# Performance work log

Hardware: AMD Instinct MI355X
Metric: run time of the kernel (lower is better)

Reference implementation:

```python
import jax, jax.numpy as jnp
import numpy as np

B, T, C = 4, 2048, 1024
H, D = 16, 64  # n_head, head_dim; H*D == C
EPS = 1e-12


def _l2norm(x):
    # matches torch F.normalize(dim=-1): x / max(||x||_2, eps)
    n = jnp.sqrt(jnp.sum(x * x, axis=-1, keepdims=True))
    return x / jnp.maximum(n, EPS)


def setup_inputs() -> dict:
    key = jax.random.key(0)
    ks = jax.random.split(key, 8)
    s = 0.02
    return {
        "x": jax.random.normal(ks[0], (B, T, C), dtype=jnp.float32),
        "Wq": jax.random.normal(ks[1], (C, C), dtype=jnp.float32) * s,
        "Wk": jax.random.normal(ks[2], (C, C), dtype=jnp.float32) * s,
        "Wv": jax.random.normal(ks[3], (C, C), dtype=jnp.float32) * s,
        "Wbeta": jax.random.normal(ks[4], (H, C), dtype=jnp.float32) * s,
        "bbeta": jnp.zeros((H,), dtype=jnp.float32),
        "Wgate": jax.random.normal(ks[5], (C, C), dtype=jnp.float32) * s,
        "Wo": jax.random.normal(ks[6], (C, C), dtype=jnp.float32) * s,
    }


def _forward(x, Wq, Wk, Wv, Wbeta, bbeta, Wgate, Wo):
    q = (x @ Wq.T).reshape(B, T, H, D)
    k = (x @ Wk.T).reshape(B, T, H, D)
    v = (x @ Wv.T).reshape(B, T, H, D)
    beta = jax.nn.sigmoid(x @ Wbeta.T + bbeta)  # (B,T,H)
    gate = jax.nn.sigmoid(x @ Wgate.T)          # (B,T,C)

    q = _l2norm(q)
    k = _l2norm(k)

    # time-major for scan: (T,B,H,D) / (T,B,H)
    qT = jnp.transpose(q, (1, 0, 2, 3))
    kT = jnp.transpose(k, (1, 0, 2, 3))
    vT = jnp.transpose(v, (1, 0, 2, 3))
    bT = jnp.transpose(beta, (1, 0, 2))

    M0 = jnp.zeros((B, H, D, D), dtype=x.dtype)

    def step(M, inp):
        q_t, k_t, v_t, b_t = inp
        o_t = jnp.einsum('bhdc,bhc->bhd', M, q_t)       # read state with q (pre-update)
        Mk = jnp.einsum('bhdc,bhc->bhd', M, k_t)
        dv = v_t - Mk                                    # delta-rule error
        M = M + b_t[..., None, None] * jnp.einsum('bhd,bhc->bhdc', dv, k_t)
        return M, o_t

    _, oT = jax.lax.scan(step, M0, (qT, kT, vT, bT))     # oT: (T,B,H,D)
    o = jnp.transpose(oT, (1, 0, 2, 3)).reshape(B, T, C)
    return (gate * o) @ Wo.T


def reference(x, Wq, Wk, Wv, Wbeta, bbeta, Wgate, Wo):
    return _forward(x, Wq, Wk, Wv, Wbeta, bbeta, Wgate, Wo)
```

## Files before the change

kernel.cpp:

```cpp
#include <hip/hip_runtime.h>
#include <cstdint>
#include <cstddef>

#define Bz 4
#define Tz 2048
#define Cz 1024
#define Hz 16
#define Dz 64
#define NTOK (Bz*Tz)
#define CHL 32
#define NCH (Tz/CHL)

typedef __attribute__((ext_vector_type(8))) short  short8;
typedef __attribute__((ext_vector_type(4))) float  floatx4;

__device__ __forceinline__ unsigned short f2bf(float x) {
  union { float f; uint32_t u; } a; a.f = x;
  uint32_t r = a.u + 0x7fffu + ((a.u >> 16) & 1u);
  return (unsigned short)(r >> 16);
}
__device__ __forceinline__ float bf2f(unsigned short u) {
  union { uint32_t i; float f; } a; a.i = ((uint32_t)u) << 16; return a.f;
}
__device__ __forceinline__ float sigmoidf_(float z) {
  return 1.0f / (1.0f + __expf(-z));
}
__device__ __forceinline__ uint32_t cvtpk_bf16(float a, float b) {
  uint32_t d;
  asm volatile("v_cvt_pk_bf16_f32 %0, %1, %2" : "=v"(d) : "v"(a), "v"(b));
  return d;
}
__device__ __forceinline__ float lo16f(uint32_t u) {
  union { uint32_t i; float f; } a; a.i = u << 16; return a.f;
}
__device__ __forceinline__ float hi16f(uint32_t u) {
  union { uint32_t i; float f; } a; a.i = u & 0xffff0000u; return a.f;
}

__device__ __forceinline__ void gload_lds16(const void* gptr, void* lptr) {
  __builtin_amdgcn_global_load_lds(
      (const __attribute__((address_space(1))) void*)(uintptr_t)gptr,
      (__attribute__((address_space(3))) void*)(uint32_t)(uintptr_t)lptr,
      16, 0, 0);
}

template<int CTRL>
__device__ __forceinline__ float dpp_addf(float x) {
  int y = __builtin_amdgcn_update_dpp(0, __float_as_int(x), CTRL, 0xF, 0xF, true);
  return x + __int_as_float(y);
}
__device__ __forceinline__ float rowsum16(float x) {
  x = dpp_addf<0xB1>(x);
  x = dpp_addf<0x4E>(x);
  x = dpp_addf<0x124>(x);
  x = dpp_addf<0x128>(x);
  return x;
}

union FragU { uint32_t u[4]; short8 s; };

__global__ __launch_bounds__(256) void cvt_bf16_kernel(const float* __restrict__ in,
                                                       unsigned short* __restrict__ out,
                                                       int n4) {
  int i = blockIdx.x * blockDim.x + threadIdx.x;
  int stride = gridDim.x * blockDim.x;
  const float4* in4 = (const float4*)in;
  ushort4* out4 = (ushort4*)out;
  for (; i < n4; i += stride) {
    float4 f = in4[i];
    ushort4 u;
    u.x = f2bf(f.x); u.y = f2bf(f.y); u.z = f2bf(f.z); u.w = f2bf(f.w);
    out4[i] = u;
  }
}

__global__ __launch_bounds__(256) void cvt_w5_kernel(
    const float* __restrict__ s0, const float* __restrict__ s1,
    const float* __restrict__ s2, const float* __restrict__ s3,
    const float* __restrict__ s4,
    unsigned short* __restrict__ d0, unsigned short* __restrict__ d1,
    unsigned short* __restrict__ d2, unsigned short* __restrict__ d3,
    unsigned short* __restrict__ d4, int n4)
{
  const int w = blockIdx.y;
  const float* s = (w == 0) ? s0 : (w == 1) ? s1 : (w == 2) ? s2 : (w == 3) ? s3 : s4;
  unsigned short* d = (w == 0) ? d0 : (w == 1) ? d1 : (w == 2) ? d2 : (w == 3) ? d3 : d4;
  int i = blockIdx.x * blockDim.x + threadIdx.x;
  if (i < n4) {
    float4 f = ((const float4*)s)[i];
    ushort4 u;
    u.x = f2bf(f.x); u.y = f2bf(f.y); u.z = f2bf(f.z); u.w = f2bf(f.w);
    ((ushort4*)d)[i] = u;
  }
}

#define VM8()  asm volatile("s_waitcnt vmcnt(8)" ::: "memory")
#define VM4()  asm volatile("s_waitcnt vmcnt(4)" ::: "memory")
#define VM0()  asm volatile("s_waitcnt vmcnt(0)" ::: "memory")
#define LGKM0() asm volatile("s_waitcnt lgkmcnt(0)" ::: "memory")
#define BARR() __builtin_amdgcn_s_barrier()

__global__ __launch_bounds__(512, 2) void gemm256_kernel(
    const unsigned short* __restrict__ A,
    const unsigned short* __restrict__ W0, const unsigned short* __restrict__ W1,
    const unsigned short* __restrict__ W2, const unsigned short* __restrict__ W3,
    void* __restrict__ O0, void* __restrict__ O1,
    void* __restrict__ O2, void* __restrict__ O3,
    int M, int N, int K, int nz_sigmoid, int norm_mask, int out_bf16)
{
  __shared__ unsigned short smem[8 * 8192];

  const int gx = gridDim.x, gz = gridDim.z;
  const int nwg = gx * gridDim.y * gz;
  int flat = (blockIdx.z * gridDim.y + blockIdx.y) * gx + blockIdx.x;
  if ((nwg & 7) == 0) flat = (flat & 7) * (nwg >> 3) + (flat >> 3);
  const int xz = gx * gz;
  const int by = flat / xz;
  const int rem = flat - by * xz;
  const int bz = rem / gx;
  const int bx = rem - bz * gx;

  const unsigned short* Bw = (bz == 0) ? W0 : (bz == 1) ? W1 : (bz == 2) ? W2 : W3;
  void* Cw = (bz == 0) ? O0 : (bz == 1) ? O1 : (bz == 2) ? O2 : O3;
  const bool act = (bz == nz_sigmoid);
  const bool donorm = (norm_mask >> bz) & 1;

  const int m0 = by * 256, n0 = bx * 256;
  const int tid = threadIdx.x;
  const int wid = tid >> 6, lane = tid & 63;
  const int wm = wid >> 2, wn = wid & 3;
  const int ml = lane & 15, kq = lane >> 4;

  const unsigned short* Ap = A  + (size_t)m0 * K;
  const unsigned short* Bp = Bw + (size_t)n0 * K;

  const int srow = wid * 16 + (lane >> 2);
  const int ss8  = ((lane & 3) ^ ((lane >> 3) & 3)) * 8;
  const int rs8  = (kq ^ ((ml >> 1) & 3)) * 8;
  const int arow = wm * 128 + ml;
  const int brow = wn * 64 + ml;

  const int NT = K >> 6;
  const int hmax = NT << 2;

  floatx4 acc[8][4];
#pragma unroll
  for (int i = 0; i < 8; ++i)
#pragma unroll
    for (int j = 0; j < 4; ++j) acc[i][j] = floatx4{0.f, 0.f, 0.f, 0.f};

#define STAGE1(hsi) do {                                                      \
    const int ht_ = (hsi) >> 2, hh_ = (hsi) & 3;                              \
    const unsigned short* p_ = (hh_ & 1) ? Bp : Ap;                           \
    const int kb_ = ht_ * 64 + (hh_ >> 1) * 32;                               \
    unsigned short* lb_ = &smem[(((ht_ & 1) << 2) + hh_) * 8192 + wid * 512]; \
    gload_lds16(p_ + (size_t)srow * K + kb_ + ss8, lb_);                      \
    gload_lds16(p_ + (size_t)(128 + srow) * K + kb_ + ss8, lb_ + 4096);       \
  } while (0)

  int hs = 0;
  for (; hs < 6 && hs < hmax; ++hs) STAGE1(hs);
  VM8();
  BARR();

#define LOAD_A(Hb, mh)                                                        \
  _Pragma("unroll") for (int i = 0; i < 4; ++i)                               \
    af[i] = *(const short8*)&Hb[(arow + (mh) * 64 + i * 16) * 32 + rs8];
#define LOAD_B(Hb)                                                            \
  _Pragma("unroll") for (int j = 0; j < 4; ++j)                               \
    bf[j] = *(const short8*)&Hb[(brow + j * 16) * 32 + rs8];
#define MFMA_Q(mh)                                                            \
  __builtin_amdgcn_s_setprio(1);                                              \
  _Pragma("unroll") for (int i = 0; i < 4; ++i)                               \
    _Pragma("unroll") for (int j = 0; j < 4; ++j)                             \
      acc[(mh) * 4 + i][j] = __builtin_amdgcn_mfma_f32_16x16x32_bf16(         \
          af[i], bf[j], acc[(mh) * 4 + i][j], 0, 0, 0);                       \
  __builtin_amdgcn_s_setprio(0);
#define STAGE_NEXT() do { if (hs < hmax) { STAGE1(hs); ++hs; } } while (0)

  short8 af[4], bf[4];
  for (int t = 0; t < NT; ++t) {
    const unsigned short* Ah0 = &smem[(((t & 1) << 2) + 0) * 8192];
    const unsigned short* Bh0 = &smem[(((t & 1) << 2) + 1) * 8192];
    const unsigned short* Ah1 = &smem[(((t & 1) << 2) + 2) * 8192];
    const unsigned short* Bh1 = &smem[(((t & 1) << 2) + 3) * 8192];

    LOAD_A(Ah0, 0); LOAD_B(Bh0);
    STAGE_NEXT();
    BARR(); LGKM0();
    MFMA_Q(0);
    BARR();

    LOAD_A(Ah0, 1);
    STAGE_NEXT();
    BARR(); LGKM0();
    MFMA_Q(1);
    if (t == NT - 1) { VM0(); } else { VM8(); }
    BARR();

    LOAD_A(Ah1, 0); LOAD_B(Bh1);
    STAGE_NEXT();
    BARR(); LGKM0();
    MFMA_Q(0);
    BARR();

    LOAD_A(Ah1, 1);
    STAGE_NEXT();
    BARR(); LGKM0();
    MFMA_Q(1);
    if (t < NT - 2) { VM8(); } else if (t == NT - 2) { VM4(); }
    BARR();
  }

  float scale[8][4];
  if (donorm) {
#pragma unroll
    for (int i = 0; i < 8; ++i) {
#pragma unroll
      for (int r = 0; r < 4; ++r) {
        float ss = 0.f;
#pragma unroll
        for (int j = 0; j < 4; ++j) ss = fmaf(acc[i][j][r], acc[i][j][r], ss);
        ss = rowsum16(ss);
        scale[i][r] = 1.0f / fmaxf(sqrtf(ss), 1e-12f);
      }
    }
  }

  const int row_base = m0 + wm * 128;
  const int col_base = n0 + wn * 64;
#pragma unroll
  for (int i = 0; i < 8; ++i) {
#pragma unroll
    for (int j = 0; j < 4; ++j) {
      const int col = col_base + j * 16 + ml;
#pragma unroll
      for (int r = 0; r < 4; ++r) {
        const int row = row_base + i * 16 + kq * 4 + r;
        float val = acc[i][j][r];
        if (donorm) val *= scale[i][r];
        if (act) val = sigmoidf_(val);
        if (out_bf16) ((unsigned short*)Cw)[(size_t)row * N + col] = f2bf(val);
        else          ((float*)Cw)[(size_t)row * N + col] = val;
      }
    }
  }
}

__global__ __launch_bounds__(256) void beta_kernel(
    const float* __restrict__ x, const float* __restrict__ Wb,
    const float* __restrict__ bb, float* __restrict__ beta_out)
{
  const int n = blockIdx.x;
  const int wid = threadIdx.x >> 6;
  const int lane = threadIdx.x & 63;
  const float* xr = x + (size_t)n * Cz;
  for (int h = wid; h < Hz; h += 4) {
    const float* wr = Wb + (size_t)h * Cz;
    float s = 0.f;
#pragma unroll 4
    for (int i = lane; i < Cz; i += 64) s = fmaf(xr[i], wr[i], s);
#pragma unroll
    for (int ofs = 32; ofs >= 1; ofs >>= 1) s += __shfl_xor(s, ofs);
    if (lane == 0) beta_out[(size_t)n * Hz + h] = sigmoidf_(s + bb[h]);
  }
}


__global__ __launch_bounds__(256) void deltachunk_phase1(
    const unsigned short* __restrict__ qb, const unsigned short* __restrict__ kb,
    const unsigned short* __restrict__ vb, const float* __restrict__ betaf,
    float* __restrict__ of,
    unsigned short* __restrict__ qtb, unsigned short* __restrict__ wbuf,
    unsigned short* __restrict__ ubuf, unsigned short* __restrict__ ktb)
{
  __shared__ unsigned short Kb[32][72], Qb[32][72], Vb[32][72];
  __shared__ float As[32][33];
  __shared__ unsigned short Sb[32][40];
  __shared__ unsigned short Us[32][72], Ws[32][72], Qts[32][72];
  __shared__ float bsh[32];

  const int bid = blockIdx.x;
  const int chain = bid & 63;
  const int chunk = bid >> 6;
  const int b = chain >> 4, h = chain & 15;
  const int tid = threadIdx.x;
  const int wid = tid >> 6, lane = tid & 63;
  const int ml = lane & 15, kq = lane >> 4;

  const size_t tok0 = (size_t)b * Tz + (size_t)chunk * CHL;
  const size_t cb = ((size_t)chain * NCH + chunk) * 2048;

  {
    const int row = tid >> 3, c8 = (tid & 7) * 8;
    const size_t ga = (tok0 + row) * Cz + h * Dz + c8;
    *(uint4*)&Qb[row][c8] = *(const uint4*)&qb[ga];
    *(uint4*)&Kb[row][c8] = *(const uint4*)&kb[ga];
    *(uint4*)&Vb[row][c8] = *(const uint4*)&vb[ga];
  }
  if (tid < 32) bsh[tid] = betaf[(tok0 + tid) * Hz + h];
  __syncthreads();

  {
    const int tr = wid & 1, tc = wid >> 1;
    floatx4 accA = {0.f,0.f,0.f,0.f}, accS = {0.f,0.f,0.f,0.f};
#pragma unroll
    for (int eh = 0; eh < 2; ++eh) {
      short8 ka = *(const short8*)&Kb[tr * 16 + ml][eh * 32 + kq * 8];
      short8 kbf = *(const short8*)&Kb[tc * 16 + ml][eh * 32 + kq * 8];
      short8 qa = *(const short8*)&Qb[tr * 16 + ml][eh * 32 + kq * 8];
      accA = __builtin_amdgcn_mfma_f32_16x16x32_bf16(ka, kbf, accA, 0, 0, 0);
      accS = __builtin_amdgcn_mfma_f32_16x16x32_bf16(qa, kbf, accS, 0, 0, 0);
    }
#pragma unroll
    for (int r = 0; r < 4; ++r) {
      int t = tr * 16 + kq * 4 + r;
      int s = tc * 16 + ml;
      As[t][s] = bsh[t] * accA[r];
      Sb[t][s] = (t > s) ? f2bf(accS[r]) : (unsigned short)0;
    }
  }
  __syncthreads();

  if (tid < 128) {
    const int j = tid;
    float x[32];
    if (j < 64) {
#pragma unroll
      for (int t = 0; t < 32; ++t) x[t] = bsh[t] * bf2f(Vb[t][j]);
    } else {
#pragma unroll
      for (int t = 0; t < 32; ++t) x[t] = bsh[t] * bf2f(Kb[t][j - 64]);
    }
#pragma unroll
    for (int t = 0; t < 31; ++t) {
      float xt = x[t];
#pragma unroll
      for (int s = t + 1; s < 32; ++s) x[s] = fmaf(-As[s][t], xt, x[s]);
    }
    if (j < 64) {
#pragma unroll
      for (int t = 0; t < 32; ++t) Us[t][j] = f2bf(x[t]);
    } else {
#pragma unroll
      for (int t = 0; t < 32; ++t) Ws[t][j - 64] = f2bf(x[t]);
    }
  }
  __syncthreads();

  {
    const int dw = wid * 16 + ml;
    FragU bu, bw;
#pragma unroll
    for (int r = 0; r < 4; ++r) {
      bu.u[r] = (uint32_t)Us[kq * 8 + 2 * r][dw] | ((uint32_t)Us[kq * 8 + 2 * r + 1][dw] << 16);
      bw.u[r] = (uint32_t)Ws[kq * 8 + 2 * r][dw] | ((uint32_t)Ws[kq * 8 + 2 * r + 1][dw] << 16);
    }
    floatx4 accO[2], accQ[2];
#pragma unroll
    for (int tt = 0; tt < 2; ++tt) { accO[tt] = floatx4{0.f,0.f,0.f,0.f}; accQ[tt] = floatx4{0.f,0.f,0.f,0.f}; }
#pragma unroll
    for (int tt = 0; tt < 2; ++tt) {
      short8 sa = *(const short8*)&Sb[tt * 16 + ml][kq * 8];
      accO[tt] = __builtin_amdgcn_mfma_f32_16x16x32_bf16(sa, bu.s, accO[tt], 0, 0, 0);
      accQ[tt] = __builtin_amdgcn_mfma_f32_16x16x32_bf16(sa, bw.s, accQ[tt], 0, 0, 0);
    }
#pragma unroll
    for (int tt = 0; tt < 2; ++tt) {
#pragma unroll
      for (int r = 0; r < 4; ++r) {
        int t = tt * 16 + kq * 4 + r;
        of[(tok0 + t) * Cz + h * Dz + dw] = accO[tt][r];
        Qts[t][dw] = f2bf(bf2f(Qb[t][dw]) - accQ[tt][r]);
      }
    }
  }

  unsigned short ktmp[8], utmp[8];
  {
    const int e = tid >> 2, tq = (tid & 3) * 8;
#pragma unroll
    for (int i2 = 0; i2 < 8; ++i2) { ktmp[i2] = Kb[tq + i2][e]; utmp[i2] = Us[tq + i2][e]; }
  }
  __syncthreads();

  {
    const int row = tid >> 3, c8 = (tid & 7) * 8;
    const size_t o16 = cb + (size_t)row * 64 + c8;
    *(uint4*)&qtb[o16]  = *(const uint4*)&Qts[row][c8];
    *(uint4*)&wbuf[o16] = *(const uint4*)&Ws[row][c8];
    const int e = tid >> 2, tq = (tid & 3) * 8;
    *(uint4*)&ktb[cb + (size_t)e * 32 + tq]  = *(const uint4*)ktmp;
    *(uint4*)&ubuf[cb + (size_t)e * 32 + tq] = *(const uint4*)utmp;
  }
}

__global__ __launch_bounds__(256, 1) void deltachunk_phase2(
    const unsigned short* __restrict__ qtb, const unsigned short* __restrict__ wbuf,
    const unsigned short* __restrict__ ubuf, const unsigned short* __restrict__ ktb,
    float* __restrict__ of)
{
  __shared__ unsigned short Gb[2][64][72];
  __shared__ unsigned short Ub[2][64][40];
  __shared__ unsigned short Kts[2][64][40];
  __shared__ unsigned short Mh[2][64][72], Ml[2][64][72];

  const int chain = blockIdx.x;
  const int b = chain >> 4, h = chain & 15;
  const int tid = threadIdx.x;
  const int wid = tid >> 6, lane = tid & 63;
  const int ml = lane & 15, kq = lane >> 4;
  const int iq = wid >> 1, jq = wid & 1;

  for (int i = tid; i < 64 * 72; i += 256) { (&Mh[0][0][0])[i] = 0; (&Ml[0][0][0])[i] = 0; }

  const int g_row = tid >> 2;
  const int g_c0  = (tid & 3) * 16;
  const int k_e   = tid >> 1;
  const int k_c0  = (tid & 1) * 16;

  const size_t cbase = (size_t)chain * NCH * 2048;

  float pre[2][2][4];
  if (iq == 0) {
#pragma unroll
    for (int u = 0; u < 2; ++u) {
      *(uint4*)&Gb[0][g_row][g_c0 + 8*u]    = *(const uint4*)&qtb[cbase + (size_t)g_row * 64 + g_c0 + 8*u];
      *(uint4*)&Gb[0][32 + g_row][g_c0 + 8*u] = *(const uint4*)&wbuf[cbase + (size_t)g_row * 64 + g_c0 + 8*u];
      *(uint4*)&Ub[0][k_e][k_c0 + 8*u]      = *(const uint4*)&ubuf[cbase + (size_t)k_e * 32 + k_c0 + 8*u];
      *(uint4*)&Kts[0][k_e][k_c0 + 8*u]     = *(const uint4*)&ktb[cbase + (size_t)k_e * 32 + k_c0 + 8*u];
    }
    const size_t t0 = (size_t)b * Tz;
#pragma unroll
    for (int ti = 0; ti < 2; ++ti)
#pragma unroll
      for (int tj = 0; tj < 2; ++tj)
#pragma unroll
        for (int r = 0; r < 4; ++r)
          pre[ti][tj][r] = of[(t0 + ti * 16 + kq * 4 + r) * Cz + h * Dz + jq * 32 + tj * 16 + ml];
  }
  __syncthreads();

  const int idxA = ((lane & 15) + 16 * ((2 * kq + 0) & 3)) * 4;
  const int idxB = ((lane & 15) + 16 * ((2 * kq + 1) & 3)) * 4;
  const bool hiKq = (kq >= 2);

  floatx4 mAcc[4][2];
#pragma unroll
  for (int a = 0; a < 4; ++a) { mAcc[a][0] = floatx4{0.f,0.f,0.f,0.f}; mAcc[a][1] = floatx4{0.f,0.f,0.f,0.f}; }

  int cbuf = 0;
  for (int c = 0; c < NCH; ++c) {
    const int nbuf = cbuf ^ 1;
    const int mr = c & 1, mw = mr ^ 1;
    const size_t tok0 = (size_t)b * Tz + (size_t)c * CHL;

    uint4 sq[2], sw[2], su[2], sk[2];
    float preN[2][2][4];
    const int cn = (c + 1 < NCH) ? c + 1 : c;
    if (iq == 0) {
      const size_t cbn = cbase + (size_t)cn * 2048;
#pragma unroll
      for (int u = 0; u < 2; ++u) {
        sq[u] = *(const uint4*)&qtb[cbn + (size_t)g_row * 64 + g_c0 + 8*u];
        sw[u] = *(const uint4*)&wbuf[cbn + (size_t)g_row * 64 + g_c0 + 8*u];
        su[u] = *(const uint4*)&ubuf[cbn + (size_t)k_e * 32 + k_c0 + 8*u];
        sk[u] = *(const uint4*)&ktb[cbn + (size_t)k_e * 32 + k_c0 + 8*u];
      }
      const size_t tkn = (size_t)b * Tz + (size_t)cn * CHL;
#pragma unroll
      for (int ti = 0; ti < 2; ++ti)
#pragma unroll
        for (int tj = 0; tj < 2; ++tj)
#pragma unroll
          for (int r = 0; r < 4; ++r)
            preN[ti][tj][r] = of[(tkn + ti * 16 + kq * 4 + r) * Cz + h * Dz + jq * 32 + tj * 16 + ml];
    }

    floatx4 g1[2][2];
#pragma unroll
    for (int ti = 0; ti < 2; ++ti)
#pragma unroll
      for (int tj = 0; tj < 2; ++tj) g1[ti][tj] = floatx4{0.f,0.f,0.f,0.f};
#pragma unroll
    for (int eh = 0; eh < 2; ++eh) {
      short8 afr0 = *(const short8*)&Gb[cbuf][iq * 32 + 0  + ml][eh * 32 + kq * 8];
      short8 afr1 = *(const short8*)&Gb[cbuf][iq * 32 + 16 + ml][eh * 32 + kq * 8];
#pragma unroll
      for (int hl = 0; hl < 2; ++hl) {
#pragma unroll
        for (int tj = 0; tj < 2; ++tj) {
          short8 bfr = hl ? *(const short8*)&Ml[mr][jq * 32 + tj * 16 + ml][eh * 32 + kq * 8]
                          : *(const short8*)&Mh[mr][jq * 32 + tj * 16 + ml][eh * 32 + kq * 8];
          g1[0][tj] = __builtin_amdgcn_mfma_f32_16x16x32_bf16(afr0, bfr, g1[0][tj], 0, 0, 0);
          g1[1][tj] = __builtin_amdgcn_mfma_f32_16x16x32_bf16(afr1, bfr, g1[1][tj], 0, 0, 0);
        }
      }
    }

    if (iq == 0) {
#pragma unroll
      for (int ti = 0; ti < 2; ++ti)
#pragma unroll
        for (int tj = 0; tj < 2; ++tj)
#pragma unroll
          for (int r = 0; r < 4; ++r)
            of[(tok0 + ti * 16 + kq * 4 + r) * Cz + h * Dz + jq * 32 + tj * 16 + ml] =
                pre[ti][tj][r] + g1[ti][tj][r];
#pragma unroll
      for (int u = 0; u < 2; ++u) {
        *(uint4*)&Gb[nbuf][g_row][g_c0 + 8*u]    = sq[u];
        *(uint4*)&Gb[nbuf][32 + g_row][g_c0 + 8*u] = sw[u];
        *(uint4*)&Ub[nbuf][k_e][k_c0 + 8*u]      = su[u];
        *(uint4*)&Kts[nbuf][k_e][k_c0 + 8*u]     = sk[u];
      }
#pragma unroll
      for (int ti = 0; ti < 2; ++ti)
#pragma unroll
        for (int tj = 0; tj < 2; ++tj)
#pragma unroll
          for (int r = 0; r < 4; ++r) pre[ti][tj][r] = preN[ti][tj][r];
    } else {
      uint32_t pkh[2][2][2], pkl[2][2][2];
#pragma unroll
      for (int ti = 0; ti < 2; ++ti) {
#pragma unroll
        for (int tj = 0; tj < 2; ++tj) {
          const int d = jq * 32 + tj * 16 + ml;
          ushort4 uu = *(const ushort4*)&Ub[cbuf][d][ti * 16 + kq * 4];
          float z0 = bf2f(uu.x) - g1[ti][tj][0];
          float z1 = bf2f(uu.y) - g1[ti][tj][1];
          float z2 = bf2f(uu.z) - g1[ti][tj][2];
          float z3 = bf2f(uu.w) - g1[ti][tj][3];
          uint32_t h01 = cvtpk_bf16(z0, z1), h23 = cvtpk_bf16(z2, z3);
          pkh[ti][tj][0] = h01; pkh[ti][tj][1] = h23;
          pkl[ti][tj][0] = cvtpk_bf16(z0 - lo16f(h01), z1 - hi16f(h01));
          pkl[ti][tj][1] = cvtpk_bf16(z2 - lo16f(h23), z3 - hi16f(h23));
        }
      }
      FragU zh[2], zl[2];
#pragma unroll
      for (int tj = 0; tj < 2; ++tj) {
#pragma unroll
        for (int s = 0; s < 4; ++s) {
          const int idx = (s < 2) ? idxA : idxB;
          const int rp = s & 1;
          int v0 = __builtin_amdgcn_ds_bpermute(idx, (int)pkh[0][tj][rp]);
          int v1 = __builtin_amdgcn_ds_bpermute(idx, (int)pkh[1][tj][rp]);
          zh[tj].u[s] = hiKq ? (uint32_t)v1 : (uint32_t)v0;
          int w0 = __builtin_amdgcn_ds_bpermute(idx, (int)pkl[0][tj][rp]);
          int w1 = __builtin_amdgcn_ds_bpermute(idx, (int)pkl[1][tj][rp]);
          zl[tj].u[s] = hiKq ? (uint32_t)w1 : (uint32_t)w0;
        }
      }
#pragma unroll
      for (int et = 0; et < 4; ++et) {
        short8 kfr = *(const short8*)&Kts[cbuf][et * 16 + ml][kq * 8];
#pragma unroll
        for (int tj = 0; tj < 2; ++tj) {
          mAcc[et][tj] = __builtin_amdgcn_mfma_f32_16x16x32_bf16(kfr, zh[tj].s, mAcc[et][tj], 0, 0, 0);
          mAcc[et][tj] = __builtin_amdgcn_mfma_f32_16x16x32_bf16(kfr, zl[tj].s, mAcc[et][tj], 0, 0, 0);
        }
      }
#pragma unroll
      for (int et = 0; et < 4; ++et) {
#pragma unroll
        for (int tj = 0; tj < 2; ++tj) {
          const int d = jq * 32 + tj * 16 + ml;
          float m0 = mAcc[et][tj][0], m1 = mAcc[et][tj][1];
          float m2 = mAcc[et][tj][2], m3 = mAcc[et][tj][3];
          uint32_t h01 = cvtpk_bf16(m0, m1), h23 = cvtpk_bf16(m2, m3);
          uint32_t l01 = cvtpk_bf16(m0 - lo16f(h01), m1 - hi16f(h01));
          uint32_t l23 = cvtpk_bf16(m2 - lo16f(h23), m3 - hi16f(h23));
          *(uint32_t*)&Mh[mw][d][et * 16 + kq * 4]     = h01;
          *(uint32_t*)&Mh[mw][d][et * 16 + kq * 4 + 2] = h23;
          *(uint32_t*)&Ml[mw][d][et * 16 + kq * 4]     = l01;
          *(uint32_t*)&Ml[mw][d][et * 16 + kq * 4 + 2] = l23;
        }
      }
    }
    __syncthreads();
    cbuf ^= 1;
  }
}

__global__ __launch_bounds__(256) void gate_mul_kernel(
    const unsigned short* __restrict__ gsig, const float* __restrict__ o,
    unsigned short* __restrict__ out, int n4)
{
  int i = blockIdx.x * blockDim.x + threadIdx.x;
  int stride = gridDim.x * blockDim.x;
  const ushort4* g4 = (const ushort4*)gsig;
  const float4* o4 = (const float4*)o;
  ushort4* out4 = (ushort4*)out;
  for (; i < n4; i += stride) {
    ushort4 gv = g4[i];
    float4 ov = o4[i];
    ushort4 u;
    u.x = f2bf(bf2f(gv.x) * ov.x);
    u.y = f2bf(bf2f(gv.y) * ov.y);
    u.z = f2bf(bf2f(gv.z) * ov.z);
    u.w = f2bf(bf2f(gv.w) * ov.w);
    out4[i] = u;
  }
}

extern "C" void kernel_launch(void* const* d_in, const int* in_sizes, int n_in,
                              void* d_out, int out_size, void* d_ws, size_t ws_size,
                              hipStream_t stream) {
  const float* x     = (const float*)d_in[0];
  const float* Wq    = (const float*)d_in[1];
  const float* Wk    = (const float*)d_in[2];
  const float* Wv    = (const float*)d_in[3];
  const float* Wbeta = (const float*)d_in[4];
  const float* bbeta = (const float*)d_in[5];
  const float* Wgate = (const float*)d_in[6];
  const float* Wo    = (const float*)d_in[7];
  float* out = (float*)d_out;

  char* ws = (char*)d_ws;
  size_t off = 0;
  auto alloc = [&](size_t bytes) -> char* {
    char* p = ws + off;
    off += (bytes + 255) & ~(size_t)255;
    return p;
  };
  unsigned short* xb  = (unsigned short*)alloc((size_t)NTOK * Cz * 2);
  unsigned short* Wqb = (unsigned short*)alloc((size_t)Cz * Cz * 2);
  unsigned short* Wkb = (unsigned short*)alloc((size_t)Cz * Cz * 2);
  unsigned short* Wvb = (unsigned short*)alloc((size_t)Cz * Cz * 2);
  unsigned short* Wgb = (unsigned short*)alloc((size_t)Cz * Cz * 2);
  unsigned short* Wob = (unsigned short*)alloc((size_t)Cz * Cz * 2);
  unsigned short* qb  = (unsigned short*)alloc((size_t)NTOK * Cz * 2);
  unsigned short* kb  = (unsigned short*)alloc((size_t)NTOK * Cz * 2);
  unsigned short* vb  = (unsigned short*)alloc((size_t)NTOK * Cz * 2);
  unsigned short* gb  = (unsigned short*)alloc((size_t)NTOK * Cz * 2);
  float* of    = (float*)alloc((size_t)NTOK * Cz * 4);
  float* betaf = (float*)alloc((size_t)NTOK * Hz * 4);
  unsigned short* qtb  = (unsigned short*)alloc((size_t)64 * NCH * 2048 * 2);
  unsigned short* wbuf = (unsigned short*)alloc((size_t)64 * NCH * 2048 * 2);
  unsigned short* ubuf = (unsigned short*)alloc((size_t)64 * NCH * 2048 * 2);
  unsigned short* ktb  = (unsigned short*)alloc((size_t)64 * NCH * 2048 * 2);
  unsigned short* ab = xb;

  const int n4x = NTOK * Cz / 4;
  const int n4w = Cz * Cz / 4;

  cvt_bf16_kernel<<<dim3(1024), dim3(256), 0, stream>>>(x, xb, n4x);
  cvt_w5_kernel<<<dim3(n4w / 256, 5), dim3(256), 0, stream>>>(
      Wq, Wk, Wv, Wgate, Wo, Wqb, Wkb, Wvb, Wgb, Wob, n4w);

  gemm256_kernel<<<dim3(Cz / 256, NTOK / 256, 4), dim3(512), 0, stream>>>(
      xb, Wqb, Wkb, Wvb, Wgb, qb, kb, vb, gb, NTOK, Cz, Cz, 3, 3, 1);

  beta_kernel<<<dim3(NTOK), dim3(256), 0, stream>>>(x, Wbeta, bbeta, betaf);

  deltachunk_phase1<<<dim3(64 * NCH), dim3(256), 0, stream>>>(
      qb, kb, vb, betaf, of, qtb, wbuf, ubuf, ktb);
  deltachunk_phase2<<<dim3(Bz * Hz), dim3(256), 0, stream>>>(qtb, wbuf, ubuf, ktb, of);

  gate_mul_kernel<<<dim3(1024), dim3(256), 0, stream>>>(gb, of, ab, n4x);

  gemm256_kernel<<<dim3(Cz / 256, NTOK / 256, 1), dim3(512), 0, stream>>>(
      ab, Wob, Wob, Wob, Wob, out, out, out, out, NTOK, Cz, Cz, -1, 0, 0);
}
```

Baseline: 411.6 us.

## Split delta-rule state recurrence across value-dim halves and defer intra-chunk add

The sequential chunk-recurrence kernel now runs two blocks per (batch, head) chain, each owning 32 of the 64 value columns of the state, which doubles the parallelism of the serial scan from 64 to 128 blocks. The inter-chunk output contribution is written to a separate buffer instead of a read-modify-write of the intra-chunk output, and the gate kernel sums the two buffers. All threads now share the next-chunk prefetch, and the barrier uses an explicit LDS wait. This adds an extra fp32 activation buffer and more memory traffic in the gate kernel, and it duplicates the Q/W/K loads across the two blocks.

Result: faster. 374.0 us (-9.2%).

```diff
diff --git a/kernel.cpp b/kernel.cpp
--- a/kernel.cpp
+++ b/kernel.cpp
@@ -395,212 +395,158 @@
   }
 }
 
-__global__ __launch_bounds__(256, 1) void deltachunk_phase2(
+__global__ __launch_bounds__(256) void deltachunk_phase2(
     const unsigned short* __restrict__ qtb, const unsigned short* __restrict__ wbuf,
     const unsigned short* __restrict__ ubuf, const unsigned short* __restrict__ ktb,
-    float* __restrict__ of)
+    float* __restrict__ o2)
 {
   __shared__ unsigned short Gb[2][64][72];
-  __shared__ unsigned short Ub[2][64][40];
+  __shared__ unsigned short Ub[2][32][40];
   __shared__ unsigned short Kts[2][64][40];
-  __shared__ unsigned short Mh[2][64][72], Ml[2][64][72];
-
-  const int chain = blockIdx.x;
+  __shared__ unsigned short Mh[2][32][72], Ml[2][32][72];
+
+  const int chain = blockIdx.x >> 1;
+  const int dh = blockIdx.x & 1;
   const int b = chain >> 4, h = chain & 15;
+  const int d0 = dh * 32;
   const int tid = threadIdx.x;
   const int wid = tid >> 6, lane = tid & 63;
   const int ml = lane & 15, kq = lane >> 4;
   const int iq = wid >> 1, jq = wid & 1;
 
-  for (int i = tid; i < 64 * 72; i += 256) { (&Mh[0][0][0])[i] = 0; (&Ml[0][0][0])[i] = 0; }
-
-  const int g_row = tid >> 2;
-  const int g_c0  = (tid & 3) * 16;
-  const int k_e   = tid >> 1;
-  const int k_c0  = (tid & 1) * 16;
-
   const size_t cbase = (size_t)chain * NCH * 2048;
 
-  float pre[2][2][4];
-  if (iq == 0) {
-#pragma unroll
-    for (int u = 0; u < 2; ++u) {
-      *(uint4*)&Gb[0][g_row][g_c0 + 8*u]    = *(const uint4*)&qtb[cbase + (size_t)g_row * 64 + g_c0 + 8*u];
-      *(uint4*)&Gb[0][32 + g_row][g_c0 + 8*u] = *(const uint4*)&wbuf[cbase + (size_t)g_row * 64 + g_c0 + 8*u];
-      *(uint4*)&Ub[0][k_e][k_c0 + 8*u]      = *(const uint4*)&ubuf[cbase + (size_t)k_e * 32 + k_c0 + 8*u];
-      *(uint4*)&Kts[0][k_e][k_c0 + 8*u]     = *(const uint4*)&ktb[cbase + (size_t)k_e * 32 + k_c0 + 8*u];
-    }
-    const size_t t0 = (size_t)b * Tz;
-#pragma unroll
-    for (int ti = 0; ti < 2; ++ti)
-#pragma unroll
-      for (int tj = 0; tj < 2; ++tj)
-#pragma unroll
-        for (int r = 0; r < 4; ++r)
-          pre[ti][tj][r] = of[(t0 + ti * 16 + kq * 4 + r) * Cz + h * Dz + jq * 32 + tj * 16 + ml];
-  }
+  const int grow = tid >> 2;
+  const int gc16 = (tid & 3) * 16;
+  const int ke   = tid >> 2;
+  const int kc8  = (tid & 3) * 8;
+  const int ue   = tid >> 3;
+  const int uc4  = (tid & 7) * 4;
+
+  const unsigned short* gsrc = (grow < 32) ? qtb : wbuf;
+  const size_t gsoff = (size_t)(grow & 31) * 64 + gc16;
+
+  {
+    *(uint4*)&Gb[0][grow][gc16]     = *(const uint4*)&gsrc[cbase + gsoff];
+    *(uint4*)&Gb[0][grow][gc16 + 8] = *(const uint4*)&gsrc[cbase + gsoff + 8];
+    *(uint4*)&Kts[0][ke][kc8]       = *(const uint4*)&ktb[cbase + (size_t)ke * 32 + kc8];
+    *(uint2*)&Ub[0][ue][uc4]        = *(const uint2*)&ubuf[cbase + (size_t)(d0 + ue) * 32 + uc4];
+  }
+  for (int i = tid; i < 32 * 72; i += 256) { (&Mh[0][0][0])[i] = 0; (&Ml[0][0][0])[i] = 0; }
   __syncthreads();
 
-  const int idxA = ((lane & 15) + 16 * ((2 * kq + 0) & 3)) * 4;
-  const int idxB = ((lane & 15) + 16 * ((2 * kq + 1) & 3)) * 4;
+  const int idxA = (ml + 16 * ((kq & 1) * 2)) * 4;
+  const int idxB = (ml + 16 * ((kq & 1) * 2 + 1)) * 4;
   const bool hiKq = (kq >= 2);
 
-  floatx4 mAcc[4][2];
-#pragma unroll
-  for (int a = 0; a < 4; ++a) { mAcc[a][0] = floatx4{0.f,0.f,0.f,0.f}; mAcc[a][1] = floatx4{0.f,0.f,0.f,0.f}; }
-
-  int cbuf = 0;
+  floatx4 mAcc[4];
+#pragma unroll
+  for (int a = 0; a < 4; ++a) mAcc[a] = floatx4{0.f, 0.f, 0.f, 0.f};
+
   for (int c = 0; c < NCH; ++c) {
-    const int nbuf = cbuf ^ 1;
+    const int cbuf = c & 1, nbuf = cbuf ^ 1;
     const int mr = c & 1, mw = mr ^ 1;
     const size_t tok0 = (size_t)b * Tz + (size_t)c * CHL;
 
-    uint4 sq[2], sw[2], su[2], sk[2];
-    float preN[2][2][4];
     const int cn = (c + 1 < NCH) ? c + 1 : c;
-    if (iq == 0) {
-      const size_t cbn = cbase + (size_t)cn * 2048;
-#pragma unroll
-      for (int u = 0; u < 2; ++u) {
-        sq[u] = *(const uint4*)&qtb[cbn + (size_t)g_row * 64 + g_c0 + 8*u];
-        sw[u] = *(const uint4*)&wbuf[cbn + (size_t)g_row * 64 + g_c0 + 8*u];
-        su[u] = *(const uint4*)&ubuf[cbn + (size_t)k_e * 32 + k_c0 + 8*u];
-        sk[u] = *(const uint4*)&ktb[cbn + (size_t)k_e * 32 + k_c0 + 8*u];
-      }
-      const size_t tkn = (size_t)b * Tz + (size_t)cn * CHL;
-#pragma unroll
-      for (int ti = 0; ti < 2; ++ti)
-#pragma unroll
-        for (int tj = 0; tj < 2; ++tj)
-#pragma unroll
-          for (int r = 0; r < 4; ++r)
-            preN[ti][tj][r] = of[(tkn + ti * 16 + kq * 4 + r) * Cz + h * Dz + jq * 32 + tj * 16 + ml];
-    }
-
-    floatx4 g1[2][2];
-#pragma unroll
-    for (int ti = 0; ti < 2; ++ti)
-#pragma unroll
-      for (int tj = 0; tj < 2; ++tj) g1[ti][tj] = floatx4{0.f,0.f,0.f,0.f};
+    const size_t cbn = cbase + (size_t)cn * 2048;
+    uint4 sg0 = *(const uint4*)&gsrc[cbn + gsoff];
+    uint4 sg1 = *(const uint4*)&gsrc[cbn + gsoff + 8];
+    uint4 sk  = *(const uint4*)&ktb[cbn + (size_t)ke * 32 + kc8];
+    uint2 su  = *(const uint2*)&ubuf[cbn + (size_t)(d0 + ue) * 32 + uc4];
+
+    floatx4 g1[2];
+    g1[0] = floatx4{0.f,0.f,0.f,0.f}; g1[1] = floatx4{0.f,0.f,0.f,0.f};
 #pragma unroll
     for (int eh = 0; eh < 2; ++eh) {
       short8 afr0 = *(const short8*)&Gb[cbuf][iq * 32 + 0  + ml][eh * 32 + kq * 8];
       short8 afr1 = *(const short8*)&Gb[cbuf][iq * 32 + 16 + ml][eh * 32 + kq * 8];
-#pragma unroll
-      for (int hl = 0; hl < 2; ++hl) {
-#pragma unroll
-        for (int tj = 0; tj < 2; ++tj) {
-          short8 bfr = hl ? *(const short8*)&Ml[mr][jq * 32 + tj * 16 + ml][eh * 32 + kq * 8]
-                          : *(const short8*)&Mh[mr][jq * 32 + tj * 16 + ml][eh * 32 + kq * 8];
-          g1[0][tj] = __builtin_amdgcn_mfma_f32_16x16x32_bf16(afr0, bfr, g1[0][tj], 0, 0, 0);
-          g1[1][tj] = __builtin_amdgcn_mfma_f32_16x16x32_bf16(afr1, bfr, g1[1][tj], 0, 0, 0);
-        }
+      short8 bh = *(const short8*)&Mh[mr][jq * 16 + ml][eh * 32 + kq * 8];
+      short8 bl = *(const short8*)&Ml[mr][jq * 16 + ml][eh * 32 + kq * 8];
+      g1[0] = __builtin_amdgcn_mfma_f32_16x16x32_bf16(afr0, bh, g1[0], 0, 0, 0);
+      g1[0] = __builtin_amdgcn_mfma_f32_16x16x32_bf16(afr0, bl, g1[0], 0, 0, 0);
+      g1[1] = __builtin_amdgcn_mfma_f32_16x16x32_bf16(afr1, bh, g1[1], 0, 0, 0);
+      g1[1] = __builtin_amdgcn_mfma_f32_16x16x32_bf16(afr1, bl, g1[1], 0, 0, 0);
+    }
+
+    if (iq == 0) {
+#pragma unroll
+      for (int ti = 0; ti < 2; ++ti)
+#pragma unroll
+        for (int r = 0; r < 4; ++r)
+          o2[(tok0 + ti * 16 + kq * 4 + r) * Cz + h * Dz + d0 + jq * 16 + ml] = g1[ti][r];
+    } else {
+      uint32_t pkh[2][2], pkl[2][2];
+#pragma unroll
+      for (int ti = 0; ti < 2; ++ti) {
+        ushort4 uu = *(const ushort4*)&Ub[cbuf][jq * 16 + ml][ti * 16 + kq * 4];
+        float z0 = bf2f(uu.x) - g1[ti][0];
+        float z1 = bf2f(uu.y) - g1[ti][1];
+        float z2 = bf2f(uu.z) - g1[ti][2];
+        float z3 = bf2f(uu.w) - g1[ti][3];
+        uint32_t h01 = cvtpk_bf16(z0, z1), h23 = cvtpk_bf16(z2, z3);
+        pkh[ti][0] = h01; pkh[ti][1] = h23;
+        pkl[ti][0] = cvtpk_bf16(z0 - lo16f(h01), z1 - hi16f(h01));
+        pkl[ti][1] = cvtpk_bf16(z2 - lo16f(h23), z3 - hi16f(h23));
       }
-    }
-
-    if (iq == 0) {
-#pragma unroll
-      for (int ti = 0; ti < 2; ++ti)
-#pragma unroll
-        for (int tj = 0; tj < 2; ++tj)
-#pragma unroll
-          for (int r = 0; r < 4; ++r)
-            of[(tok0 + ti * 16 + kq * 4 + r) * Cz + h * Dz + jq * 32 + tj * 16 + ml] =
-                pre[ti][tj][r] + g1[ti][tj][r];
-#pragma unroll
-      for (int u = 0; u < 2; ++u) {
-        *(uint4*)&Gb[nbuf][g_row][g_c0 + 8*u]    = sq[u];
-        *(uint4*)&Gb[nbuf][32 + g_row][g_c0 + 8*u] = sw[u];
-        *(uint4*)&Ub[nbuf][k_e][k_c0 + 8*u]      = su[u];
-        *(uint4*)&Kts[nbuf][k_e][k_c0 + 8*u]     = sk[u];
-      }
-#pragma unroll
-      for (int ti = 0; ti < 2; ++ti)
-#pragma unroll
-        for (int tj = 0; tj < 2; ++tj)
-#pragma unroll
-          for (int r = 0; r < 4; ++r) pre[ti][tj][r] = preN[ti][tj][r];
-    } else {
-      uint32_t pkh[2][2][2], pkl[2][2][2];
-#pragma unroll
-      for (int ti = 0; ti < 2; ++ti) {
-#pragma unroll
-        for (int tj = 0; tj < 2; ++tj) {
-          const int d = jq * 32 + tj * 16 + ml;
-          ushort4 uu = *(const ushort4*)&Ub[cbuf][d][ti * 16 + kq * 4];
-          float z0 = bf2f(uu.x) - g1[ti][tj][0];
-          float z1 = bf2f(uu.y) - g1[ti][tj][1];
-          float z2 = bf2f(uu.z) - g1[ti][tj][2];
-          float z3 = bf2f(uu.w) - g1[ti][tj][3];
-          uint32_t h01 = cvtpk_bf16(z0, z1), h23 = cvtpk_bf16(z2, z3);
-          pkh[ti][tj][0] = h01; pkh[ti][tj][1] = h23;
-          pkl[ti][tj][0] = cvtpk_bf16(z0 - lo16f(h01), z1 - hi16f(h01));
-          pkl[ti][tj][1] = cvtpk_bf16(z2 - lo16f(h23), z3 - hi16f(h23));
-        }
-      }
-      FragU zh[2], zl[2];
-#pragma unroll
-      for (int tj = 0; tj < 2; ++tj) {
-#pragma unroll
-        for (int s = 0; s < 4; ++s) {
-          const int idx = (s < 2) ? idxA : idxB;
-          const int rp = s & 1;
-          int v0 = __builtin_amdgcn_ds_bpermute(idx, (int)pkh[0][tj][rp]);
-          int v1 = __builtin_amdgcn_ds_bpermute(idx, (int)pkh[1][tj][rp]);
-          zh[tj].u[s] = hiKq ? (uint32_t)v1 : (uint32_t)v0;
-          int w0 = __builtin_amdgcn_ds_bpermute(idx, (int)pkl[0][tj][rp]);
-          int w1 = __builtin_amdgcn_ds_bpermute(idx, (int)pkl[1][tj][rp]);
-          zl[tj].u[s] = hiKq ? (uint32_t)w1 : (uint32_t)w0;
-        }
+      FragU zh, zl;
+#pragma unroll
+      for (int s = 0; s < 4; ++s) {
+        const int idx = (s < 2) ? idxA : idxB;
+        const int rp = s & 1;
+        int v0 = __builtin_amdgcn_ds_bpermute(idx, (int)pkh[0][rp]);
+        int v1 = __builtin_amdgcn_ds_bpermute(idx, (int)pkh[1][rp]);
+        zh.u[s] = hiKq ? (uint32_t)v1 : (uint32_t)v0;
+        int w0 = __builtin_amdgcn_ds_bpermute(idx, (int)pkl[0][rp]);
+        int w1 = __builtin_amdgcn_ds_bpermute(idx, (int)pkl[1][rp]);
+        zl.u[s] = hiKq ? (uint32_t)w1 : (uint32_t)w0;
       }
 #pragma unroll
       for (int et = 0; et < 4; ++et) {
         short8 kfr = *(const short8*)&Kts[cbuf][et * 16 + ml][kq * 8];
-#pragma unroll
-        for (int tj = 0; tj < 2; ++tj) {
-          mAcc[et][tj] = __builtin_amdgcn_mfma_f32_16x16x32_bf16(kfr, zh[tj].s, mAcc[et][tj], 0, 0, 0);
-          mAcc[et][tj] = __builtin_amdgcn_mfma_f32_16x16x32_bf16(kfr, zl[tj].s, mAcc[et][tj], 0, 0, 0);
-        }
+        mAcc[et] = __builtin_amdgcn_mfma_f32_16x16x32_bf16(kfr, zh.s, mAcc[et], 0, 0, 0);
+        mAcc[et] = __builtin_amdgcn_mfma_f32_16x16x32_bf16(kfr, zl.s, mAcc[et], 0, 0, 0);
       }
 #pragma unroll
       for (int et = 0; et < 4; ++et) {
-#pragma unroll
-        for (int tj = 0; tj < 2; ++tj) {
-          const int d = jq * 32 + tj * 16 + ml;
-          float m0 = mAcc[et][tj][0], m1 = mAcc[et][tj][1];
-          float m2 = mAcc[et][tj][2], m3 = mAcc[et][tj][3];
-          uint32_t h01 = cvtpk_bf16(m0, m1), h23 = cvtpk_bf16(m2, m3);
-          uint32_t l01 = cvtpk_bf16(m0 - lo16f(h01), m1 - hi16f(h01));
-          uint32_t l23 = cvtpk_bf16(m2 - lo16f(h23), m3 - hi16f(h23));
-          *(uint32_t*)&Mh[mw][d][et * 16 + kq * 4]     = h01;
-          *(uint32_t*)&Mh[mw][d][et * 16 + kq * 4 + 2] = h23;
-          *(uint32_t*)&Ml[mw][d][et * 16 + kq * 4]     = l01;
-          *(uint32_t*)&Ml[mw][d][et * 16 + kq * 4 + 2] = l23;
-        }
+        float m0 = mAcc[et][0], m1 = mAcc[et][1], m2 = mAcc[et][2], m3 = mAcc[et][3];
+        uint32_t h01 = cvtpk_bf16(m0, m1), h23 = cvtpk_bf16(m2, m3);
+        uint32_t l01 = cvtpk_bf16(m0 - lo16f(h01), m1 - hi16f(h01));
+        uint32_t l23 = cvtpk_bf16(m2 - lo16f(h23), m3 - hi16f(h23));
+        *(uint2*)&Mh[mw][jq * 16 + ml][et * 16 + kq * 4] = make_uint2(h01, h23);
+        *(uint2*)&Ml[mw][jq * 16 + ml][et * 16 + kq * 4] = make_uint2(l01, l23);
       }
     }
-    __syncthreads();
-    cbuf ^= 1;
+
+    *(uint4*)&Gb[nbuf][grow][gc16]     = sg0;
+    *(uint4*)&Gb[nbuf][grow][gc16 + 8] = sg1;
+    *(uint4*)&Kts[nbuf][ke][kc8]       = sk;
+    *(uint2*)&Ub[nbuf][ue][uc4]        = su;
+
+    LGKM0();
+    BARR();
   }
 }
 
 __global__ __launch_bounds__(256) void gate_mul_kernel(
     const unsigned short* __restrict__ gsig, const float* __restrict__ o,
-    unsigned short* __restrict__ out, int n4)
+    const float* __restrict__ o2v, unsigned short* __restrict__ out, int n4)
 {
   int i = blockIdx.x * blockDim.x + threadIdx.x;
   int stride = gridDim.x * blockDim.x;
   const ushort4* g4 = (const ushort4*)gsig;
   const float4* o4 = (const float4*)o;
+  const float4* p4 = (const float4*)o2v;
   ushort4* out4 = (ushort4*)out;
   for (; i < n4; i += stride) {
     ushort4 gv = g4[i];
     float4 ov = o4[i];
+    float4 pv = p4[i];
     ushort4 u;
-    u.x = f2bf(bf2f(gv.x) * ov.x);
-    u.y = f2bf(bf2f(gv.y) * ov.y);
-    u.z = f2bf(bf2f(gv.z) * ov.z);
-    u.w = f2bf(bf2f(gv.w) * ov.w);
+    u.x = f2bf(bf2f(gv.x) * (ov.x + pv.x));
+    u.y = f2bf(bf2f(gv.y) * (ov.y + pv.y));
+    u.z = f2bf(bf2f(gv.z) * (ov.z + pv.z));
+    u.w = f2bf(bf2f(gv.w) * (ov.w + pv.w));
     out4[i] = u;
   }
 }
@@ -636,6 +582,7 @@
   unsigned short* vb  = (unsigned short*)alloc((size_t)NTOK * Cz * 2);
   unsigned short* gb  = (unsigned short*)alloc((size_t)NTOK * Cz * 2);
   float* of    = (float*)alloc((size_t)NTOK * Cz * 4);
+  float* o2    = (float*)alloc((size_t)NTOK * Cz * 4);
   float* betaf = (float*)alloc((size_t)NTOK * Hz * 4);
   unsigned short* qtb  = (unsigned short*)alloc((size_t)64 * NCH * 2048 * 2);
   unsigned short* wbuf = (unsigned short*)alloc((size_t)64 * NCH * 2048 * 2);
@@ -657,9 +604,9 @@
 
   deltachunk_phase1<<<dim3(64 * NCH), dim3(256), 0, stream>>>(
       qb, kb, vb, betaf, of, qtb, wbuf, ubuf, ktb);
-  deltachunk_phase2<<<dim3(Bz * Hz), dim3(256), 0, stream>>>(qtb, wbuf, ubuf, ktb, of);
-
-  gate_mul_kernel<<<dim3(1024), dim3(256), 0, stream>>>(gb, of, ab, n4x);
+  deltachunk_phase2<<<dim3(128), dim3(256), 0, stream>>>(qtb, wbuf, ubuf, ktb, o2);
+
+  gate_mul_kernel<<<dim3(1024), dim3(256), 0, stream>>>(gb, of, o2, ab, n4x);
 
   gemm256_kernel<<<dim3(Cz / 256, NTOK / 256, 1), dim3(512), 0, stream>>>(
       ab, Wob, Wob, Wob, Wob, out, out, out, out, NTOK, Cz, Cz, -1, 0, 0);
```
